# Kernel optimization log

Hardware: AMD Instinct MI355X
Metric: run time of the kernel (lower is better)

## Reference

```python
import jax, jax.numpy as jnp
import numpy as np

B, T, D = 32, 2048, 128


def setup_inputs() -> dict:
    key = jax.random.key(0)
    k1, k2, k3 = jax.random.split(key, 3)
    values = jax.random.normal(k1, (B, T, D), dtype=jnp.float32)
    # monotonically increasing per-feature timestamps (irregular sampling)
    times = jnp.cumsum(jax.random.uniform(k2, (B, T, D), dtype=jnp.float32), axis=1)
    mask = jax.random.randint(k3, (B, T, D), 0, 2) > 0  # True = observed
    return {"values": values, "times": times, "mask": mask}


def _fill(x, t, mask):
    """Parallel forward fill (LOCF) and backward fill (NOCB) of x and t.

    Replaces the serial Keras RNN scan with cummax/cummin over observation
    indices followed by a gather. Matches ForwardCell semantics:
      forward : x init 0, t init times[:, 0, :]
      backward: x init 0, t init max(times, axis=1)
    """
    Tn = x.shape[1]
    ar = jnp.broadcast_to(jnp.arange(Tn, dtype=jnp.int32)[None, :, None], x.shape)
    # ---- forward fill ----
    fidx = jax.lax.cummax(jnp.where(mask, ar, -1), axis=1)  # last observed idx
    fvalid = fidx >= 0
    fi = jnp.clip(fidx, 0, Tn - 1)
    x_last = jnp.where(fvalid, jnp.take_along_axis(x, fi, axis=1), 0.0)
    t_last = jnp.where(fvalid, jnp.take_along_axis(t, fi, axis=1), t[:, :1, :])
    # ---- backward fill ----
    bidx = jax.lax.cummin(jnp.where(mask, ar, Tn), axis=1, reverse=True)  # next observed idx
    bvalid = bidx < Tn
    bi = jnp.clip(bidx, 0, Tn - 1)
    x_next = jnp.where(bvalid, jnp.take_along_axis(x, bi, axis=1), 0.0)
    t_next = jnp.where(bvalid, jnp.take_along_axis(t, bi, axis=1),
                       jnp.max(t, axis=1, keepdims=True))
    return x_last, t_last, x_next, t_next


def reference(values, times, mask):
    x_last, t_last, x_next, t_next = _fill(values, times, mask)
    denom = t_next - t_last
    num = x_last * (t_next - times) + x_next * (times - t_last)
    safe = denom != 0.0
    x_itp = num / jnp.where(safe, denom, 1.0)
    x_itp = jnp.where(safe & jnp.isfinite(x_itp), x_itp, 0.0)  # nan/inf -> 0
    return jnp.where(mask, values, x_itp)
```

## Files before the change

### kernel.cpp

```cpp
#include <hip/hip_runtime.h>
#include <math.h>

constexpr int B  = 32;
constexpr int T  = 2048;
constexpr int D  = 128;
constexpr int C  = 16;
constexpr int NC = T / C;

__global__ __launch_bounds__(256)
void linterp_kernel(const float* __restrict__ values,
                    const float* __restrict__ times,
                    const int*   __restrict__ mask,
                    float*       __restrict__ out)
{
    const int gid   = blockIdx.x * 256 + threadIdx.x;
    const int d     = gid & (D - 1);
    const int chunk = (gid >> 7) & (NC - 1);
    const int b     = gid >> 14;

    const int seq_base = b * T * D + d;
    const int t0i      = chunk * C;

    float v[C], tm[C];
    unsigned int mbits = 0;
#pragma unroll
    for (int i = 0; i < C; ++i) {
        const int off = seq_base + (t0i + i) * D;
        v[i]  = values[off];
        tm[i] = times[off];
        mbits |= (mask[off] != 0 ? 1u : 0u) << i;
    }

    const float t_first = times[seq_base];
    const float t_lastT = times[seq_base + (T - 1) * D];

    float fx = 0.f, ft = t_first;
    if (chunk > 0) {
        unsigned int pb = 0;
#pragma unroll
        for (int i = 0; i < C; ++i) {
            const int off = seq_base + (t0i - C + i) * D;
            pb |= (mask[off] != 0 ? 1u : 0u) << i;
        }
        if (pb != 0u) {
            const int idx = 31 - __builtin_clz(pb);
            const int off = seq_base + (t0i - C + idx) * D;
            fx = values[off]; ft = times[off];
        } else {
            for (int j = t0i - C - 1; j >= 0; --j) {
                const int off = seq_base + j * D;
                if (mask[off] != 0) { fx = values[off]; ft = times[off]; break; }
            }
        }
    }

    float bx = 0.f, bt = t_lastT;
    if (chunk < NC - 1) {
        unsigned int nb = 0;
#pragma unroll
        for (int i = 0; i < C; ++i) {
            const int off = seq_base + (t0i + C + i) * D;
            nb |= (mask[off] != 0 ? 1u : 0u) << i;
        }
        if (nb != 0u) {
            const int idx = __builtin_ctz(nb);
            const int off = seq_base + (t0i + C + idx) * D;
            bx = values[off]; bt = times[off];
        } else {
            for (int j = t0i + 2 * C; j < T; ++j) {
                const int off = seq_base + j * D;
                if (mask[off] != 0) { bx = values[off]; bt = times[off]; break; }
            }
        }
    }

    float xl[C], tl[C];
#pragma unroll
    for (int i = 0; i < C; ++i) {
        if ((mbits >> i) & 1u) { fx = v[i]; ft = tm[i]; }
        xl[i] = fx;
        tl[i] = ft;
    }

#pragma unroll
    for (int i = C - 1; i >= 0; --i) {
        const bool obs = (mbits >> i) & 1u;
        if (obs) { bx = v[i]; bt = tm[i]; }
        const float denom = bt - tl[i];
        const float num   = xl[i] * (bt - tm[i]) + bx * (tm[i] - tl[i]);
        const bool  safe  = (denom != 0.f);
        float xi = num / (safe ? denom : 1.f);
        xi = (safe && isfinite(xi)) ? xi : 0.f;
        out[seq_base + (t0i + i) * D] = obs ? v[i] : xi;
    }
}

extern "C" void kernel_launch(void* const* d_in, const int* in_sizes, int n_in,
                              void* d_out, int out_size, void* d_ws, size_t ws_size,
                              hipStream_t stream)
{
    const float* values = (const float*)d_in[0];
    const float* times  = (const float*)d_in[1];
    const int*   mask   = (const int*)d_in[2];
    float*       out    = (float*)d_out;

    const int total_threads = B * NC * D;
    linterp_kernel<<<total_threads / 256, 256, 0, stream>>>(values, times, mask, out);
}
```

Before: 134.0 us.

## Rewrite as wave-cooperative software-pipelined fill with float4 loads and shuffles

Replaces the one-thread-per-16-step-chunk kernel with a wave-level design. Each wave covers a 16-feature by 256-step segment in 64-step tiles and loads values, times and mask as float4/int4. Within-wave forward and backward carries are resolved with ballot and shuffle instead of each thread rescanning its neighbour's chunk. Loads are triple-buffered so the next tile is in flight while the current one is processed, which targets the redundant halo mask reads and scalar memory traffic of the old kernel. The cost is much higher register pressure (launch bounds 256,2) and more complex, macro-heavy code.

```diff
diff --git a/kernel.cpp b/kernel.cpp
--- a/kernel.cpp
+++ b/kernel.cpp
@@ -4,94 +4,215 @@
 constexpr int B  = 32;
 constexpr int T  = 2048;
 constexpr int D  = 128;
-constexpr int C  = 16;
-constexpr int NC = T / C;
-
-__global__ __launch_bounds__(256)
-void linterp_kernel(const float* __restrict__ values,
-                    const float* __restrict__ times,
-                    const int*   __restrict__ mask,
-                    float*       __restrict__ out)
+constexpr int TS = 64;
+constexpr int NT = 4;
+constexpr int WD = 16;
+
+__global__ __launch_bounds__(256, 2)
+void interp_pipe_kernel(const float* __restrict__ values,
+                       const float* __restrict__ times,
+                       const int*   __restrict__ mask,
+                       float*       __restrict__ out)
 {
-    const int gid   = blockIdx.x * 256 + threadIdx.x;
-    const int d     = gid & (D - 1);
-    const int chunk = (gid >> 7) & (NC - 1);
-    const int b     = gid >> 14;
-
-    const int seq_base = b * T * D + d;
-    const int t0i      = chunk * C;
-
-    float v[C], tm[C];
-    unsigned int mbits = 0;
+    const int tid  = threadIdx.x;
+    const int lane = tid & 63;
+    const int g    = lane >> 2;
+    const int q    = lane & 3;
+    const int waveId = (blockIdx.x << 2) | (tid >> 6);
+    const int db  = waveId & 7;
+    const int seg = (waveId >> 3) & 7;
+    const int b   = waveId >> 6;
+    const int d0  = db * WD + q * 4;
+    const int s0  = seg * (NT * TS);
+    const size_t bbase = (size_t)b * T * D;
+    const unsigned long long colmask = 0x1111111111111111ull << q;
+
+    float4 v4[3][4]; float4 t4[3][4]; int4 m4[3][4];
+    float Slv[2][4], Slt[2][4], Sfv[2][4], Sft[2][4];
+    unsigned long long Gb[2][4];
+    unsigned mbits[2][4];
+    float Fx[4], Ft[4];
+
+#define VCc(BK,i,j) ((&v4[BK][i].x)[j])
+#define TCc(BK,i,j) ((&t4[BK][i].x)[j])
+#define MCc(BK,i,j) ((&m4[BK][i].x)[j])
+
+#define LOADT(BK, st_) do { \
+    const size_t base_ = bbase + (size_t)((st_) + g * 4) * D + d0; \
+    _Pragma("unroll") \
+    for (int i_ = 0; i_ < 4; ++i_) { \
+        v4[BK][i_] = *reinterpret_cast<const float4*>(values + base_ + (size_t)i_ * D); \
+        t4[BK][i_] = *reinterpret_cast<const float4*>(times  + base_ + (size_t)i_ * D); \
+        m4[BK][i_] = *reinterpret_cast<const int4*>(mask    + base_ + (size_t)i_ * D); \
+    } } while (0)
+
+#define SUMMT(BK, SL) do { \
+    _Pragma("unroll") \
+    for (int j_ = 0; j_ < 4; ++j_) { \
+        unsigned mm_ = 0; \
+        _Pragma("unroll") \
+        for (int i_ = 0; i_ < 4; ++i_) mm_ |= (MCc(BK,i_,j_) != 0 ? 1u : 0u) << i_; \
+        mbits[SL][j_] = mm_; \
+        float a_ = 0.f, c_ = 0.f, e_ = 0.f, h_ = 0.f; \
+        _Pragma("unroll") \
+        for (int i_ = 0; i_ < 4; ++i_) \
+            if ((mm_ >> i_) & 1u) { a_ = VCc(BK,i_,j_); c_ = TCc(BK,i_,j_); } \
+        _Pragma("unroll") \
+        for (int i_ = 3; i_ >= 0; --i_) \
+            if ((mm_ >> i_) & 1u) { e_ = VCc(BK,i_,j_); h_ = TCc(BK,i_,j_); } \
+        Slv[SL][j_] = a_; Slt[SL][j_] = c_; \
+        Sfv[SL][j_] = e_; Sft[SL][j_] = h_; \
+        Gb[SL][j_]  = __ballot(mm_ != 0u); \
+    } } while (0)
+
+#define FILL_INTERP(BK, j_, mbk_, cfx_, cft_, cbx_, cbt_) do { \
+    float xl_[4], tlv_[4]; float cf_ = cfx_, ctv_ = cft_; \
+    _Pragma("unroll") \
+    for (int i_ = 0; i_ < 4; ++i_) { \
+        if ((mbk_ >> i_) & 1u) { cf_ = VCc(BK,i_,j_); ctv_ = TCc(BK,i_,j_); } \
+        xl_[i_] = cf_; tlv_[i_] = ctv_; } \
+    float cb_ = cbx_, cbt2_ = cbt_; \
+    _Pragma("unroll") \
+    for (int i_ = 3; i_ >= 0; --i_) { \
+        const bool obs_ = (mbk_ >> i_) & 1u; \
+        if (obs_) { cb_ = VCc(BK,i_,j_); cbt2_ = TCc(BK,i_,j_); } \
+        const float den_ = cbt2_ - tlv_[i_]; \
+        const float num_ = xl_[i_] * (cbt2_ - TCc(BK,i_,j_)) + cb_ * (TCc(BK,i_,j_) - tlv_[i_]); \
+        const bool safe_ = (den_ != 0.f); \
+        float xi_ = num_ / (safe_ ? den_ : 1.f); \
+        xi_ = (safe_ && isfinite(xi_)) ? xi_ : 0.f; \
+        VCc(BK,i_,j_) = obs_ ? VCc(BK,i_,j_) : xi_; } \
+    } while (0)
+
+#define STORET(BK, K) do { \
+    float* orow_ = out + bbase + (size_t)(s0 + (K) * TS + g * 4) * D + d0; \
+    _Pragma("unroll") \
+    for (int i_ = 0; i_ < 4; ++i_) \
+        *reinterpret_cast<float4*>(orow_ + (size_t)i_ * D) = v4[BK][i_]; \
+    } while (0)
+
+#define PROCN(K, BK, SK, SN) do { \
+    _Pragma("unroll") \
+    for (int j_ = 0; j_ < 4; ++j_) { \
+        const int dj_ = d0 + j_; \
+        const unsigned long long col_   = Gb[SK][j_] & colmask; \
+        const unsigned long long below_ = col_ & ((1ull << lane) - 1ull); \
+        const unsigned long long above_ = col_ & ~((2ull << lane) - 1ull); \
+        const unsigned long long colN_  = Gb[SN][j_] & colmask; \
+        const int rF_ = below_ ? (63 - __builtin_clzll(below_)) : lane; \
+        const int rB_ = above_ ? __builtin_ctzll(above_) : lane; \
+        const int rN_ = colN_  ? __builtin_ctzll(colN_)  : lane; \
+        const int rU_ = col_   ? (63 - __builtin_clzll(col_)) : lane; \
+        const float gLV_ = __shfl(Slv[SK][j_], rF_, 64); \
+        const float gLT_ = __shfl(Slt[SK][j_], rF_, 64); \
+        const float gFV_ = __shfl(Sfv[SK][j_], rB_, 64); \
+        const float gFT_ = __shfl(Sft[SK][j_], rB_, 64); \
+        const float nFV_ = __shfl(Sfv[SN][j_], rN_, 64); \
+        const float nFT_ = __shfl(Sft[SN][j_], rN_, 64); \
+        const float uLV_ = __shfl(Slv[SK][j_], rU_, 64); \
+        const float uLT_ = __shfl(Slt[SK][j_], rU_, 64); \
+        const float cfx_ = below_ ? gLV_ : Fx[j_]; \
+        const float cft_ = below_ ? gLT_ : Ft[j_]; \
+        float cbx_, cbt_; \
+        if (above_)      { cbx_ = gFV_; cbt_ = gFT_; } \
+        else if (colN_)  { cbx_ = nFV_; cbt_ = nFT_; } \
+        else {  \
+            bool fnd_ = false; cbx_ = 0.f; cbt_ = 0.f; \
+            for (int st_ = s0 + ((K) + 2) * TS; st_ < T; ++st_) { \
+                if (mask[bbase + (size_t)st_ * D + dj_] != 0) { \
+                    const size_t o_ = bbase + (size_t)st_ * D + dj_; \
+                    cbx_ = values[o_]; cbt_ = times[o_]; fnd_ = true; break; } } \
+            if (!fnd_) { cbx_ = 0.f; cbt_ = times[bbase + (size_t)(T - 1) * D + dj_]; } \
+        } \
+        const unsigned mbk_ = mbits[SK][j_]; \
+        FILL_INTERP(BK, j_, mbk_, cfx_, cft_, cbx_, cbt_); \
+        if (col_) { Fx[j_] = uLV_; Ft[j_] = uLT_; } \
+    } \
+    STORET(BK, K); } while (0)
+
+    LOADT(0, s0);
+    int4 hp4; hp4.x = 0; hp4.y = 0; hp4.z = 0; hp4.w = 0;
+    int4 hn4; hn4.x = 0; hn4.y = 0; hn4.z = 0; hn4.w = 0;
+    const bool haveHp = (seg > 0), haveHn = (seg < 7);
+    if (haveHp) hp4 = *reinterpret_cast<const int4*>(
+        mask + bbase + (size_t)(s0 - 16 + g) * D + db * WD + q * 4);
+    if (haveHn) hn4 = *reinterpret_cast<const int4*>(
+        mask + bbase + (size_t)(s0 + NT * TS + g) * D + db * WD + q * 4);
+    LOADT(1, s0 + TS);
+    SUMMT(0, 0);
+
 #pragma unroll
-    for (int i = 0; i < C; ++i) {
-        const int off = seq_base + (t0i + i) * D;
-        v[i]  = values[off];
-        tm[i] = times[off];
-        mbits |= (mask[off] != 0 ? 1u : 0u) << i;
-    }
-
-    const float t_first = times[seq_base];
-    const float t_lastT = times[seq_base + (T - 1) * D];
-
-    float fx = 0.f, ft = t_first;
-    if (chunk > 0) {
-        unsigned int pb = 0;
-#pragma unroll
-        for (int i = 0; i < C; ++i) {
-            const int off = seq_base + (t0i - C + i) * D;
-            pb |= (mask[off] != 0 ? 1u : 0u) << i;
-        }
-        if (pb != 0u) {
-            const int idx = 31 - __builtin_clz(pb);
-            const int off = seq_base + (t0i - C + idx) * D;
-            fx = values[off]; ft = times[off];
+    for (int j = 0; j < 4; ++j) {
+        const int dj = d0 + j;
+        const unsigned long long hp = __ballot(haveHp && (((&hp4.x)[j]) != 0));
+        const unsigned long long hcol = hp & colmask;
+        if (hcol) {
+            const int st = s0 - 16 + ((63 - __builtin_clzll(hcol)) >> 2);
+            const size_t o = bbase + (size_t)st * D + dj;
+            Fx[j] = values[o]; Ft[j] = times[o];
+        } else if (haveHp) {
+            bool fnd = false; Fx[j] = 0.f; Ft[j] = 0.f;
+            for (int st = s0 - 17; st >= 0; --st) {
+                if (mask[bbase + (size_t)st * D + dj] != 0) {
+                    const size_t o = bbase + (size_t)st * D + dj;
+                    Fx[j] = values[o]; Ft[j] = times[o]; fnd = true; break; }
+            }
+            if (!fnd) { Fx[j] = 0.f; Ft[j] = times[bbase + dj]; }
         } else {
-            for (int j = t0i - C - 1; j >= 0; --j) {
-                const int off = seq_base + j * D;
-                if (mask[off] != 0) { fx = values[off]; ft = times[off]; break; }
-            }
+            Fx[j] = 0.f; Ft[j] = times[bbase + dj];
         }
     }
 
-    float bx = 0.f, bt = t_lastT;
-    if (chunk < NC - 1) {
-        unsigned int nb = 0;
+    LOADT(2, s0 + 2 * TS);
+    SUMMT(1, 1);
+    PROCN(0, 0, 0, 1);
+
+    LOADT(0, s0 + 3 * TS);
+    SUMMT(2, 0);
+    PROCN(1, 1, 1, 0);
+
+    SUMMT(0, 1);
+    PROCN(2, 2, 0, 1);
+
+    {
+        const int K = 3, BK = 0, SK = 1;
+        (void)K;
 #pragma unroll
-        for (int i = 0; i < C; ++i) {
-            const int off = seq_base + (t0i + C + i) * D;
-            nb |= (mask[off] != 0 ? 1u : 0u) << i;
+        for (int j_ = 0; j_ < 4; ++j_) {
+            const int dj_ = d0 + j_;
+            const unsigned long long col_   = Gb[SK][j_] & colmask;
+            const unsigned long long below_ = col_ & ((1ull << lane) - 1ull);
+            const unsigned long long above_ = col_ & ~((2ull << lane) - 1ull);
+            const int rF_ = below_ ? (63 - __builtin_clzll(below_)) : lane;
+            const int rB_ = above_ ? __builtin_ctzll(above_) : lane;
+            const float gLV_ = __shfl(Slv[SK][j_], rF_, 64);
+            const float gLT_ = __shfl(Slt[SK][j_], rF_, 64);
+            const float gFV_ = __shfl(Sfv[SK][j_], rB_, 64);
+            const float gFT_ = __shfl(Sft[SK][j_], rB_, 64);
+            const unsigned long long hn = __ballot(haveHn && (((&hn4.x)[j_]) != 0));
+            const unsigned long long hcol_ = hn & colmask;
+            const float cfx_ = below_ ? gLV_ : Fx[j_];
+            const float cft_ = below_ ? gLT_ : Ft[j_];
+            float cbx_, cbt_;
+            if (above_) { cbx_ = gFV_; cbt_ = gFT_; }
+            else if (hcol_) {
+                const int st_ = s0 + NT * TS + ((int)__builtin_ctzll(hcol_) >> 2);
+                const size_t o_ = bbase + (size_t)st_ * D + dj_;
+                cbx_ = values[o_]; cbt_ = times[o_];
+            } else {
+                bool fnd_ = false; cbx_ = 0.f; cbt_ = 0.f;
+                const int start_ = haveHn ? (s0 + NT * TS + 16) : T;
+                for (int st_ = start_; st_ < T; ++st_) {
+                    if (mask[bbase + (size_t)st_ * D + dj_] != 0) {
+                        const size_t o_ = bbase + (size_t)st_ * D + dj_;
+                        cbx_ = values[o_]; cbt_ = times[o_]; fnd_ = true; break; }
+                }
+                if (!fnd_) { cbx_ = 0.f; cbt_ = times[bbase + (size_t)(T - 1) * D + dj_]; }
+            }
+            const unsigned mbk_ = mbits[SK][j_];
+            FILL_INTERP(BK, j_, mbk_, cfx_, cft_, cbx_, cbt_);
         }
-        if (nb != 0u) {
-            const int idx = __builtin_ctz(nb);
-            const int off = seq_base + (t0i + C + idx) * D;
-            bx = values[off]; bt = times[off];
-        } else {
-            for (int j = t0i + 2 * C; j < T; ++j) {
-                const int off = seq_base + j * D;
-                if (mask[off] != 0) { bx = values[off]; bt = times[off]; break; }
-            }
-        }
-    }
-
-    float xl[C], tl[C];
-#pragma unroll
-    for (int i = 0; i < C; ++i) {
-        if ((mbits >> i) & 1u) { fx = v[i]; ft = tm[i]; }
-        xl[i] = fx;
-        tl[i] = ft;
-    }
-
-#pragma unroll
-    for (int i = C - 1; i >= 0; --i) {
-        const bool obs = (mbits >> i) & 1u;
-        if (obs) { bx = v[i]; bt = tm[i]; }
-        const float denom = bt - tl[i];
-        const float num   = xl[i] * (bt - tm[i]) + bx * (tm[i] - tl[i]);
-        const bool  safe  = (denom != 0.f);
-        float xi = num / (safe ? denom : 1.f);
-        xi = (safe && isfinite(xi)) ? xi : 0.f;
-        out[seq_base + (t0i + i) * D] = obs ? v[i] : xi;
+        STORET(BK, 3);
     }
 }
 
@@ -104,6 +225,6 @@
     const int*   mask   = (const int*)d_in[2];
     float*       out    = (float*)d_out;
 
-    const int total_threads = B * NC * D;
-    linterp_kernel<<<total_threads / 256, 256, 0, stream>>>(values, times, mask, out);
+    const int blocks = (B * (T / (NT * TS)) * (D / WD) * 64) / 256;
+    interp_pipe_kernel<<<blocks, 256, 0, stream>>>(values, times, mask, out);
 }
```

Measured after the change: 140.8 us. 5.1% more time.
